# Optimization experiments

Hardware: AMD Instinct MI355X
Metric: run time of the kernel (lower is better)

Reference implementation:

```python
import jax, jax.numpy as jnp
import numpy as np

T = 2048          # sequence length
B = 1             # batch (forced by out.squeeze(1))
H = 2048          # hidden_size == input_size
L = 2             # num_layers
V = 128           # num_letters
TEMPERATURE = 1.0


def _lstm_layer(x, h0, c0, W_ih, W_hh, b_ih, b_hh):
    # x: [T, B, H_in], h0/c0: [B, H], W_ih: [4H, H_in], W_hh: [4H, H]
    b = b_ih + b_hh

    def step(carry, x_t):
        h, c = carry
        gates = x_t @ W_ih.T + h @ W_hh.T + b            # [B, 4H]
        i, f, g, o = jnp.split(gates, 4, axis=-1)        # torch gate order i,f,g,o
        i = jax.nn.sigmoid(i)
        f = jax.nn.sigmoid(f)
        g = jnp.tanh(g)
        o = jax.nn.sigmoid(o)
        c = f * c + i * g
        h = o * jnp.tanh(c)
        return (h, c), h

    (hT, cT), ys = jax.lax.scan(step, (h0, c0), x)       # ys: [T, B, H]
    return ys, hT, cT


def setup_inputs() -> dict:
    key = jax.random.key(0)
    ks = jax.random.split(key, 10)
    s = 1.0 / np.sqrt(H)  # torch default uniform init bound
    u = lambda k, shape: jax.random.uniform(k, shape, jnp.float32, -s, s)
    return {
        "x": jax.random.normal(ks[0], (T, B, H), jnp.float32),
        "h0": jnp.zeros((L, B, H), jnp.float32),
        "c0": jnp.zeros((L, B, H), jnp.float32),
        "W_ih": u(ks[1], (L, 4 * H, H)),
        "W_hh": u(ks[2], (L, 4 * H, H)),
        "b_ih": u(ks[3], (L, 4 * H)),
        "b_hh": u(ks[4], (L, 4 * H)),
        "fc_w": u(ks[5], (V, H)),
        "fc_b": u(ks[6], (V,)),
    }


def reference(x, h0, c0, W_ih, W_hh, b_ih, b_hh, fc_w, fc_b):
    out = x
    h_n, c_n = [], []
    for l in range(L):  # fixed small layer loop (dropout=0.1 is identity in eval)
        out, hT, cT = _lstm_layer(out, h0[l], c0[l], W_ih[l], W_hh[l], b_ih[l], b_hh[l])
        h_n.append(hT)
        c_n.append(cT)
    h_n = jnp.stack(h_n)
    c_n = jnp.stack(c_n)
    logits = out[:, 0, :] @ fc_w.T + fc_b                 # squeeze(1) -> [T, V]
    logp = jax.nn.log_softmax(logits / TEMPERATURE, axis=1)
    return logp, (h_n, c_n)
```

## Files before the change

### kernel.cpp

```cpp
#include <hip/hip_runtime.h>
#include <hip/hip_fp16.h>

#define T_LEN 2048
#define HID   2048
#define G4    8192
#define NV    128

typedef _Float16 h2_t __attribute__((ext_vector_type(2)));

__device__ __forceinline__ float uph(unsigned u) {
  return __half2float(__ushort_as_half((unsigned short)(u & 0xffffu)));
}
__device__ __forceinline__ unsigned pkh(float h, unsigned tag) {
  return (tag << 16) | (unsigned)__half_as_ushort(__float2half_rn(h));
}
__device__ __forceinline__ h2_t pk2(float a, float bb) {
  return __builtin_bit_cast(h2_t, __builtin_amdgcn_cvt_pkrtz(a, bb));
}

__device__ __forceinline__ uint4 ld_sc16(const unsigned* p) {
  uint4 r;
  asm volatile("global_load_dwordx4 %0, %1, off sc0 sc1\n\ts_waitcnt vmcnt(0)"
               : "=v"(r) : "v"(p) : "memory");
  return r;
}
__device__ __forceinline__ void ld_sc16x2(const unsigned* p0, const unsigned* p1,
                                          uint4& r0, uint4& r1) {
  asm volatile("global_load_dwordx4 %0, %2, off sc0 sc1\n\t"
               "global_load_dwordx4 %1, %3, off sc0 sc1\n\t"
               "s_waitcnt vmcnt(0)"
               : "=v"(r0), "=v"(r1) : "v"(p0), "v"(p1) : "memory");
}

__device__ __forceinline__ float fsigmoid(float x) {
  return __builtin_amdgcn_rcpf(1.f + __expf(-x));
}
__device__ __forceinline__ float ftanh(float x) {
  return 2.f * __builtin_amdgcn_rcpf(1.f + __expf(-2.f * x)) - 1.f;
}

__global__ __launch_bounds__(256, 2) void gemm_bias(
    const float* __restrict__ A, const float* __restrict__ B,
    const float* __restrict__ b1, const float* __restrict__ b2,
    float* __restrict__ C)
{
  const int N = 8192, K = 2048;
  __shared__ float As[32][68];
  __shared__ float Bs[32][68];
  const int tid = threadIdx.x;
  const int tx = tid & 15, ty = tid >> 4;
  const int row0 = blockIdx.y * 64, col0 = blockIdx.x * 64;
  const int lk = (tid & 7) * 4, lr = tid >> 3;
  float acc[4][4] = {};
  for (int k0 = 0; k0 < K; k0 += 32) {
    float4 a0 = *(const float4*)&A[(size_t)(row0 + lr)      * K + k0 + lk];
    float4 a1 = *(const float4*)&A[(size_t)(row0 + lr + 32) * K + k0 + lk];
    float4 bb0 = *(const float4*)&B[(size_t)(col0 + lr)      * K + k0 + lk];
    float4 bb1 = *(const float4*)&B[(size_t)(col0 + lr + 32) * K + k0 + lk];
    __syncthreads();
    As[lk+0][lr] = a0.x;  As[lk+1][lr] = a0.y;  As[lk+2][lr] = a0.z;  As[lk+3][lr] = a0.w;
    As[lk+0][lr+32] = a1.x; As[lk+1][lr+32] = a1.y; As[lk+2][lr+32] = a1.z; As[lk+3][lr+32] = a1.w;
    Bs[lk+0][lr] = bb0.x; Bs[lk+1][lr] = bb0.y; Bs[lk+2][lr] = bb0.z; Bs[lk+3][lr] = bb0.w;
    Bs[lk+0][lr+32] = bb1.x; Bs[lk+1][lr+32] = bb1.y; Bs[lk+2][lr+32] = bb1.z; Bs[lk+3][lr+32] = bb1.w;
    __syncthreads();
    #pragma unroll
    for (int kk = 0; kk < 32; ++kk) {
      float4 av = *(const float4*)&As[kk][ty * 4];
      float4 bv = *(const float4*)&Bs[kk][tx * 4];
      float am[4] = {av.x, av.y, av.z, av.w};
      float bm[4] = {bv.x, bv.y, bv.z, bv.w};
      #pragma unroll
      for (int i = 0; i < 4; ++i)
        #pragma unroll
        for (int j = 0; j < 4; ++j)
          acc[i][j] = fmaf(am[i], bm[j], acc[i][j]);
    }
  }
  #pragma unroll
  for (int i = 0; i < 4; ++i) {
    const int r = row0 + ty * 4 + i;
    #pragma unroll
    for (int j = 0; j < 4; ++j) {
      const int cc = col0 + tx * 4 + j;
      C[(size_t)r * N + cc] = acc[i][j] + b1[cc] + b2[cc];
    }
  }
}

__global__ __launch_bounds__(512, 2) void lstm_rec2(
    const float* __restrict__ Whh0,
    const float* __restrict__ Wih1,
    const float* __restrict__ Whh1,
    const float* __restrict__ G,
    const float* __restrict__ bih1, const float* __restrict__ bhh1,
    const float* __restrict__ h0v,
    const float* __restrict__ c0v,
    unsigned* HbufP0, unsigned* HbufP1,
    float* __restrict__ hn, float* __restrict__ cn)
{
  const int b = blockIdx.x;
  const int tid = threadIdx.x;
  const int w = tid >> 6;
  const int lane = tid & 63;
  const int j = b * 8 + w;
  __shared__ unsigned hs0[2][HID / 2];
  __shared__ unsigned hs1[2][HID / 2];

  h2_t wreg0[4][16], wregI[4][16], wregH[4][16];
  #pragma unroll
  for (int g = 0; g < 4; ++g) {
    const float* r0 = Whh0 + (size_t)(g * 2048 + j) * 2048 + 2 * lane;
    #pragma unroll
    for (int it = 0; it < 16; ++it) {
      float2 v = *(const float2*)(r0 + 128 * it);
      wreg0[g][it] = pk2(v.x, v.y);
    }
  }
  #pragma unroll
  for (int g = 0; g < 4; ++g) {
    const float* rI = Wih1 + (size_t)(g * 2048 + j) * 2048 + 2 * lane;
    #pragma unroll
    for (int it = 0; it < 16; ++it) {
      float2 v = *(const float2*)(rI + 128 * it);
      wregI[g][it] = pk2(v.x, v.y);
    }
  }
  #pragma unroll
  for (int g = 0; g < 4; ++g) {
    const float* rH = Whh1 + (size_t)(g * 2048 + j) * 2048 + 2 * lane;
    #pragma unroll
    for (int it = 0; it < 16; ++it) {
      float2 v = *(const float2*)(rH + 128 * it);
      wregH[g][it] = pk2(v.x, v.y);
    }
  }
  float bias1[4];
  #pragma unroll
  for (int g = 0; g < 4; ++g)
    bias1[g] = bih1[g * 2048 + j] + bhh1[g * 2048 + j];

  float c0val = c0v[j];
  float c1val = c0v[HID + j];
  float h0last = 0.f, h1last = 0.f;

  if (tid < 8) {
    __hip_atomic_store(&HbufP0[b * 8 + tid], pkh(h0v[b * 8 + tid], 0u),
                       __ATOMIC_RELAXED, __HIP_MEMORY_SCOPE_AGENT);
    __hip_atomic_store(&HbufP1[b * 8 + tid], pkh(h0v[HID + b * 8 + tid], 0u),
                       __ATOMIC_RELAXED, __HIP_MEMORY_SCOPE_AGENT);
  }

  for (int r = 1; r <= T_LEN + 1; ++r) {
    const bool doL0 = (r <= T_LEN);
    float gpre = (doL0 && lane < 4) ? G[(size_t)(r - 1) * G4 + lane * 2048 + j] : 0.f;

    const unsigned want0 = (unsigned)(r - 1);
    const unsigned* src0 = HbufP0 + (size_t)(r - 1) * HID + 4 * tid;
    uint4 u0, u1;
    if (r >= 2) {
      const unsigned want1 = (unsigned)(r - 2);
      const unsigned* src1 = HbufP1 + (size_t)(r - 2) * HID + 4 * tid;
      ld_sc16x2(src0, src1, u0, u1);
      int sp = 0;
      while (!(((u1.x >> 16) == want1) & ((u1.y >> 16) == want1) &
               ((u1.z >> 16) == want1) & ((u1.w >> 16) == want1))) {
        if (++sp > 4) __builtin_amdgcn_s_sleep(1);
        if (sp > (1 << 20)) break;
        u1 = ld_sc16(src1);
      }
      unsigned* row1 = hs1[r & 1];
      *(uint2*)&row1[2 * tid] = make_uint2((u1.x & 0xffffu) | (u1.y << 16),
                                           (u1.z & 0xffffu) | (u1.w << 16));
    } else {
      u0 = ld_sc16(src0);
    }
    {
      int sp = 0;
      while (!(((u0.x >> 16) == want0) & ((u0.y >> 16) == want0) &
               ((u0.z >> 16) == want0) & ((u0.w >> 16) == want0))) {
        if (++sp > 4) __builtin_amdgcn_s_sleep(1);
        if (sp > (1 << 20)) break;
        u0 = ld_sc16(src0);
      }
    }
    unsigned* row0 = hs0[r & 1];
    *(uint2*)&row0[2 * tid] = make_uint2((u0.x & 0xffffu) | (u0.y << 16),
                                         (u0.z & 0xffffu) | (u0.w << 16));
    __syncthreads();

    if (doL0) {
      const unsigned* hr = hs0[r & 1];
      float a0 = 0.f, a1 = 0.f, a2 = 0.f, a3 = 0.f;
      #pragma unroll
      for (int it = 0; it < 16; ++it) {
        h2_t hv = __builtin_bit_cast(h2_t, hr[lane + 64 * it]);
        a0 = __builtin_amdgcn_fdot2(wreg0[0][it], hv, a0, false);
        a1 = __builtin_amdgcn_fdot2(wreg0[1][it], hv, a1, false);
        a2 = __builtin_amdgcn_fdot2(wreg0[2][it], hv, a2, false);
        a3 = __builtin_amdgcn_fdot2(wreg0[3][it], hv, a3, false);
      }
      #pragma unroll
      for (int off = 32; off > 0; off >>= 1) {
        a0 += __shfl_xor(a0, off, 64);
        a1 += __shfl_xor(a1, off, 64);
        a2 += __shfl_xor(a2, off, 64);
        a3 += __shfl_xor(a3, off, 64);
      }
      float g0 = __shfl(gpre, 0, 64), g1 = __shfl(gpre, 1, 64);
      float g2 = __shfl(gpre, 2, 64), g3 = __shfl(gpre, 3, 64);
      float ig = fsigmoid(a0 + g0);
      float fg = fsigmoid(a1 + g1);
      float gg = ftanh(a2 + g2);
      float og = fsigmoid(a3 + g3);
      c0val = fg * c0val + ig * gg;
      h0last = og * ftanh(c0val);
      if (lane == 0)
        __hip_atomic_store(&HbufP0[(size_t)r * HID + j], pkh(h0last, (unsigned)r),
                           __ATOMIC_RELAXED, __HIP_MEMORY_SCOPE_AGENT);
    }

    if (r >= 2) {
      const unsigned* xr = hs0[r & 1];
      const unsigned* hr = hs1[r & 1];
      float a0 = 0.f, a1 = 0.f, a2 = 0.f, a3 = 0.f;
      #pragma unroll
      for (int it = 0; it < 16; ++it) {
        h2_t xv = __builtin_bit_cast(h2_t, xr[lane + 64 * it]);
        a0 = __builtin_amdgcn_fdot2(wregI[0][it], xv, a0, false);
        a1 = __builtin_amdgcn_fdot2(wregI[1][it], xv, a1, false);
        a2 = __builtin_amdgcn_fdot2(wregI[2][it], xv, a2, false);
        a3 = __builtin_amdgcn_fdot2(wregI[3][it], xv, a3, false);
        h2_t hv = __builtin_bit_cast(h2_t, hr[lane + 64 * it]);
        a0 = __builtin_amdgcn_fdot2(wregH[0][it], hv, a0, false);
        a1 = __builtin_amdgcn_fdot2(wregH[1][it], hv, a1, false);
        a2 = __builtin_amdgcn_fdot2(wregH[2][it], hv, a2, false);
        a3 = __builtin_amdgcn_fdot2(wregH[3][it], hv, a3, false);
      }
      #pragma unroll
      for (int off = 32; off > 0; off >>= 1) {
        a0 += __shfl_xor(a0, off, 64);
        a1 += __shfl_xor(a1, off, 64);
        a2 += __shfl_xor(a2, off, 64);
        a3 += __shfl_xor(a3, off, 64);
      }
      float ig = fsigmoid(a0 + bias1[0]);
      float fg = fsigmoid(a1 + bias1[1]);
      float gg = ftanh(a2 + bias1[2]);
      float og = fsigmoid(a3 + bias1[3]);
      c1val = fg * c1val + ig * gg;
      h1last = og * ftanh(c1val);
      if (lane == 0)
        __hip_atomic_store(&HbufP1[(size_t)(r - 1) * HID + j],
                           pkh(h1last, (unsigned)(r - 1)),
                           __ATOMIC_RELAXED, __HIP_MEMORY_SCOPE_AGENT);
    }
  }
  if (lane == 0) {
    hn[j] = h0last;       cn[j] = c0val;
    hn[HID + j] = h1last; cn[HID + j] = c1val;
  }
}

__global__ __launch_bounds__(128) void fc_lsm(
    const unsigned* __restrict__ Hrows,
    const float* __restrict__ fcw,
    const float* __restrict__ fcb,
    float* __restrict__ out)
{
  const int t = blockIdx.x;
  const int v = threadIdx.x;
  __shared__ float hs[HID];
  __shared__ float red[4];
  const unsigned* hrow = Hrows + (size_t)t * HID;
  for (int q = v; q < HID / 4; q += 128) {
    uint4 uv = *(const uint4*)&hrow[q * 4];
    hs[q * 4 + 0] = uph(uv.x); hs[q * 4 + 1] = uph(uv.y);
    hs[q * 4 + 2] = uph(uv.z); hs[q * 4 + 3] = uph(uv.w);
  }
  __syncthreads();
  const float* wrow = fcw + (size_t)v * HID;
  float acc = fcb[v];
  #pragma unroll 4
  for (int k = 0; k < HID; k += 4) {
    float4 wv = *(const float4*)&wrow[k];
    acc = fmaf(wv.x, hs[k],     acc);
    acc = fmaf(wv.y, hs[k + 1], acc);
    acc = fmaf(wv.z, hs[k + 2], acc);
    acc = fmaf(wv.w, hs[k + 3], acc);
  }
  float m = acc;
  #pragma unroll
  for (int off = 32; off > 0; off >>= 1) m = fmaxf(m, __shfl_xor(m, off, 64));
  if ((v & 63) == 0) red[v >> 6] = m;
  __syncthreads();
  m = fmaxf(red[0], red[1]);
  float e = expf(acc - m), s = e;
  #pragma unroll
  for (int off = 32; off > 0; off >>= 1) s += __shfl_xor(s, off, 64);
  if ((v & 63) == 0) red[2 + (v >> 6)] = s;
  __syncthreads();
  s = red[2] + red[3];
  out[(size_t)t * NV + v] = (acc - m) - logf(s);
}

extern "C" void kernel_launch(void* const* d_in, const int* in_sizes, int n_in,
                              void* d_out, int out_size, void* d_ws, size_t ws_size,
                              hipStream_t stream) {
  const float* x   = (const float*)d_in[0];
  const float* h0  = (const float*)d_in[1];
  const float* c0  = (const float*)d_in[2];
  const float* Wih = (const float*)d_in[3];
  const float* Whh = (const float*)d_in[4];
  const float* bih = (const float*)d_in[5];
  const float* bhh = (const float*)d_in[6];
  const float* fcw = (const float*)d_in[7];
  const float* fcb = (const float*)d_in[8];
  float* out = (float*)d_out;

  char* ws = (char*)d_ws;
  float*    G      = (float*)(ws);
  unsigned* HbufP0 = (unsigned*)(ws + 67108864);
  unsigned* HbufP1 = (unsigned*)(ws + 67108864 + 16785408);

  dim3 ggrid(G4 / 64, T_LEN / 64);

  gemm_bias<<<ggrid, 256, 0, stream>>>(x, Wih, bih, bhh, G);
  lstm_rec2<<<256, 512, 0, stream>>>(Whh, Wih + (size_t)G4 * HID,
                                     Whh + (size_t)G4 * HID, G,
                                     bih + G4, bhh + G4, h0, c0,
                                     HbufP0, HbufP1,
                                     out + 262144, out + 266240);
  fc_lsm<<<T_LEN, 128, 0, stream>>>(HbufP1 + HID, fcw, fcb, out);
}
```

Measured before the change: 12.08 ms.

## Replace per-element tagged hidden-state words with packed rows plus per-block flags

Each block now gathers its eight hidden values in shared memory and writes them as one packed fp16 row chunk, then sets a per-block flag word. Before, every value carried its own step tag in the upper half of a 32-bit word. Consumers poll 256 flags with one wavefront per layer and then bulk-load the packed rows, which halves the hidden-state traffic and drops per-element tag checks. In exchange it adds a flag-zeroing kernel, extra __syncthreads per step, and a store-then-flag ordering that relies on the waitcnt inside st_sc16.

```diff
diff --git a/kernel.cpp b/kernel.cpp
--- a/kernel.cpp
+++ b/kernel.cpp
@@ -7,12 +7,18 @@
 #define NV    128
 
 typedef _Float16 h2_t __attribute__((ext_vector_type(2)));
-
-__device__ __forceinline__ float uph(unsigned u) {
+typedef unsigned u32x4 __attribute__((ext_vector_type(4)));
+
+__device__ __forceinline__ float uplo(unsigned u) {
   return __half2float(__ushort_as_half((unsigned short)(u & 0xffffu)));
 }
-__device__ __forceinline__ unsigned pkh(float h, unsigned tag) {
-  return (tag << 16) | (unsigned)__half_as_ushort(__float2half_rn(h));
+__device__ __forceinline__ float uphi(unsigned u) {
+  return __half2float(__ushort_as_half((unsigned short)(u >> 16)));
+}
+__device__ __forceinline__ unsigned pku(float a, float b) {
+  unsigned lo = (unsigned)__half_as_ushort(__float2half_rn(a));
+  unsigned hi = (unsigned)__half_as_ushort(__float2half_rn(b));
+  return lo | (hi << 16);
 }
 __device__ __forceinline__ h2_t pk2(float a, float bb) {
   return __builtin_bit_cast(h2_t, __builtin_amdgcn_cvt_pkrtz(a, bb));
@@ -24,12 +30,13 @@
                : "=v"(r) : "v"(p) : "memory");
   return r;
 }
-__device__ __forceinline__ void ld_sc16x2(const unsigned* p0, const unsigned* p1,
-                                          uint4& r0, uint4& r1) {
-  asm volatile("global_load_dwordx4 %0, %2, off sc0 sc1\n\t"
-               "global_load_dwordx4 %1, %3, off sc0 sc1\n\t"
-               "s_waitcnt vmcnt(0)"
-               : "=v"(r0), "=v"(r1) : "v"(p0), "v"(p1) : "memory");
+__device__ __forceinline__ void st_sc16(unsigned* p, u32x4 v) {
+  asm volatile("global_store_dwordx4 %0, %1, off sc0 sc1\n\ts_waitcnt vmcnt(0)"
+               :: "v"(p), "v"(v) : "memory");
+}
+__device__ __forceinline__ void st_sc4(unsigned* p, unsigned v) {
+  asm volatile("global_store_dword %0, %1, off sc0 sc1"
+               :: "v"(p), "v"(v) : "memory");
 }
 
 __device__ __forceinline__ float fsigmoid(float x) {
@@ -37,6 +44,25 @@
 }
 __device__ __forceinline__ float ftanh(float x) {
   return 2.f * __builtin_amdgcn_rcpf(1.f + __expf(-2.f * x)) - 1.f;
+}
+
+__device__ __forceinline__ void poll_flags(const unsigned* f, unsigned want,
+                                           int lane) {
+  const unsigned* p = f + 4 * lane;
+  int sp = 0;
+  for (;;) {
+    uint4 u = ld_sc16(p);
+    bool ok = (u.x == want) & (u.y == want) & (u.z == want) & (u.w == want);
+    if (__all(ok)) break;
+    if (++sp > 8) __builtin_amdgcn_s_sleep(1);
+    if (sp > (1 << 15)) break;
+  }
+}
+
+__global__ __launch_bounds__(256) void zero_flags(unsigned* f, int n4) {
+  u32x4 z = {0u, 0u, 0u, 0u};
+  for (int i = blockIdx.x * 256 + threadIdx.x; i < n4; i += gridDim.x * 256)
+    st_sc16(f + 4 * (size_t)i, z);
 }
 
 __global__ __launch_bounds__(256, 2) void gemm_bias(
@@ -87,7 +113,7 @@
   }
 }
 
-__global__ __launch_bounds__(512, 2) void lstm_rec2(
+__global__ __launch_bounds__(512) void lstm_rec2(
     const float* __restrict__ Whh0,
     const float* __restrict__ Wih1,
     const float* __restrict__ Whh1,
@@ -95,7 +121,8 @@
     const float* __restrict__ bih1, const float* __restrict__ bhh1,
     const float* __restrict__ h0v,
     const float* __restrict__ c0v,
-    unsigned* HbufP0, unsigned* HbufP1,
+    unsigned* Hrow0, unsigned* Hrow1,
+    unsigned* flags0, unsigned* flags1,
     float* __restrict__ hn, float* __restrict__ cn)
 {
   const int b = blockIdx.x;
@@ -105,6 +132,7 @@
   const int j = b * 8 + w;
   __shared__ unsigned hs0[2][HID / 2];
   __shared__ unsigned hs1[2][HID / 2];
+  __shared__ float hloc0[8], hloc1[8];
 
   h2_t wreg0[4][16], wregI[4][16], wregH[4][16];
   #pragma unroll
@@ -143,49 +171,40 @@
   float c1val = c0v[HID + j];
   float h0last = 0.f, h1last = 0.f;
 
-  if (tid < 8) {
-    __hip_atomic_store(&HbufP0[b * 8 + tid], pkh(h0v[b * 8 + tid], 0u),
-                       __ATOMIC_RELAXED, __HIP_MEMORY_SCOPE_AGENT);
-    __hip_atomic_store(&HbufP1[b * 8 + tid], pkh(h0v[HID + b * 8 + tid], 0u),
-                       __ATOMIC_RELAXED, __HIP_MEMORY_SCOPE_AGENT);
+  if (tid == 0) {
+    u32x4 P = {pku(h0v[b*8+0], h0v[b*8+1]),
+               pku(h0v[b*8+2], h0v[b*8+3]),
+               pku(h0v[b*8+4], h0v[b*8+5]),
+               pku(h0v[b*8+6], h0v[b*8+7])};
+    st_sc16(Hrow0 + b * 4, P);
+    st_sc4(flags0 + b, 1u);
+  }
+  if (tid == 64) {
+    u32x4 P = {pku(h0v[HID+b*8+0], h0v[HID+b*8+1]),
+               pku(h0v[HID+b*8+2], h0v[HID+b*8+3]),
+               pku(h0v[HID+b*8+4], h0v[HID+b*8+5]),
+               pku(h0v[HID+b*8+6], h0v[HID+b*8+7])};
+    st_sc16(Hrow1 + b * 4, P);
+    st_sc4(flags1 + b, 1u);
   }
 
   for (int r = 1; r <= T_LEN + 1; ++r) {
     const bool doL0 = (r <= T_LEN);
+    const bool doL1 = (r >= 2);
     float gpre = (doL0 && lane < 4) ? G[(size_t)(r - 1) * G4 + lane * 2048 + j] : 0.f;
 
-    const unsigned want0 = (unsigned)(r - 1);
-    const unsigned* src0 = HbufP0 + (size_t)(r - 1) * HID + 4 * tid;
-    uint4 u0, u1;
-    if (r >= 2) {
-      const unsigned want1 = (unsigned)(r - 2);
-      const unsigned* src1 = HbufP1 + (size_t)(r - 2) * HID + 4 * tid;
-      ld_sc16x2(src0, src1, u0, u1);
-      int sp = 0;
-      while (!(((u1.x >> 16) == want1) & ((u1.y >> 16) == want1) &
-               ((u1.z >> 16) == want1) & ((u1.w >> 16) == want1))) {
-        if (++sp > 4) __builtin_amdgcn_s_sleep(1);
-        if (sp > (1 << 20)) break;
-        u1 = ld_sc16(src1);
-      }
-      unsigned* row1 = hs1[r & 1];
-      *(uint2*)&row1[2 * tid] = make_uint2((u1.x & 0xffffu) | (u1.y << 16),
-                                           (u1.z & 0xffffu) | (u1.w << 16));
-    } else {
-      u0 = ld_sc16(src0);
-    }
-    {
-      int sp = 0;
-      while (!(((u0.x >> 16) == want0) & ((u0.y >> 16) == want0) &
-               ((u0.z >> 16) == want0) & ((u0.w >> 16) == want0))) {
-        if (++sp > 4) __builtin_amdgcn_s_sleep(1);
-        if (sp > (1 << 20)) break;
-        u0 = ld_sc16(src0);
-      }
-    }
-    unsigned* row0 = hs0[r & 1];
-    *(uint2*)&row0[2 * tid] = make_uint2((u0.x & 0xffffu) | (u0.y << 16),
-                                         (u0.z & 0xffffu) | (u0.w << 16));
+    if (w == 0)        poll_flags(flags0 + (size_t)(r - 1) * 256, (unsigned)r, lane);
+    else if (w == 1 && doL1) poll_flags(flags1 + (size_t)(r - 2) * 256, (unsigned)(r - 1), lane);
+    __syncthreads();
+
+    if (tid < 256) {
+      uint4 u = ld_sc16(Hrow0 + (size_t)(r - 1) * 1024 + 4 * tid);
+      *(uint4*)&hs0[r & 1][4 * tid] = u;
+    } else if (doL1) {
+      const int q = tid - 256;
+      uint4 u = ld_sc16(Hrow1 + (size_t)(r - 2) * 1024 + 4 * q);
+      *(uint4*)&hs1[r & 1][4 * q] = u;
+    }
     __syncthreads();
 
     if (doL0) {
@@ -214,12 +233,17 @@
       float og = fsigmoid(a3 + g3);
       c0val = fg * c0val + ig * gg;
       h0last = og * ftanh(c0val);
-      if (lane == 0)
-        __hip_atomic_store(&HbufP0[(size_t)r * HID + j], pkh(h0last, (unsigned)r),
-                           __ATOMIC_RELAXED, __HIP_MEMORY_SCOPE_AGENT);
-    }
-
-    if (r >= 2) {
+      if (lane == 0) hloc0[w] = h0last;
+    }
+    __syncthreads();
+    if (doL0 && tid == 0) {
+      u32x4 P = {pku(hloc0[0], hloc0[1]), pku(hloc0[2], hloc0[3]),
+                 pku(hloc0[4], hloc0[5]), pku(hloc0[6], hloc0[7])};
+      st_sc16(Hrow0 + (size_t)r * 1024 + b * 4, P);
+      st_sc4(flags0 + (size_t)r * 256 + b, (unsigned)(r + 1));
+    }
+
+    if (doL1) {
       const unsigned* xr = hs0[r & 1];
       const unsigned* hr = hs1[r & 1];
       float a0 = 0.f, a1 = 0.f, a2 = 0.f, a3 = 0.f;
@@ -249,10 +273,14 @@
       float og = fsigmoid(a3 + bias1[3]);
       c1val = fg * c1val + ig * gg;
       h1last = og * ftanh(c1val);
-      if (lane == 0)
-        __hip_atomic_store(&HbufP1[(size_t)(r - 1) * HID + j],
-                           pkh(h1last, (unsigned)(r - 1)),
-                           __ATOMIC_RELAXED, __HIP_MEMORY_SCOPE_AGENT);
+      if (lane == 0) hloc1[w] = h1last;
+    }
+    __syncthreads();
+    if (doL1 && tid == 64) {
+      u32x4 P = {pku(hloc1[0], hloc1[1]), pku(hloc1[2], hloc1[3]),
+                 pku(hloc1[4], hloc1[5]), pku(hloc1[6], hloc1[7])};
+      st_sc16(Hrow1 + (size_t)(r - 1) * 1024 + b * 4, P);
+      st_sc4(flags1 + (size_t)(r - 1) * 256 + b, (unsigned)r);
     }
   }
   if (lane == 0) {
@@ -271,11 +299,13 @@
   const int v = threadIdx.x;
   __shared__ float hs[HID];
   __shared__ float red[4];
-  const unsigned* hrow = Hrows + (size_t)t * HID;
-  for (int q = v; q < HID / 4; q += 128) {
+  const unsigned* hrow = Hrows + (size_t)t * 1024;
+  for (int q = v; q < 256; q += 128) {
     uint4 uv = *(const uint4*)&hrow[q * 4];
-    hs[q * 4 + 0] = uph(uv.x); hs[q * 4 + 1] = uph(uv.y);
-    hs[q * 4 + 2] = uph(uv.z); hs[q * 4 + 3] = uph(uv.w);
+    hs[q*8+0] = uplo(uv.x); hs[q*8+1] = uphi(uv.x);
+    hs[q*8+2] = uplo(uv.y); hs[q*8+3] = uphi(uv.y);
+    hs[q*8+4] = uplo(uv.z); hs[q*8+5] = uphi(uv.z);
+    hs[q*8+6] = uplo(uv.w); hs[q*8+7] = uphi(uv.w);
   }
   __syncthreads();
   const float* wrow = fcw + (size_t)v * HID;
@@ -319,8 +349,13 @@
 
   char* ws = (char*)d_ws;
   float*    G      = (float*)(ws);
-  unsigned* HbufP0 = (unsigned*)(ws + 67108864);
-  unsigned* HbufP1 = (unsigned*)(ws + 67108864 + 16785408);
+  unsigned* Hrow0  = (unsigned*)(ws + 67108864);
+  unsigned* Hrow1  = (unsigned*)(ws + 67108864 + 8392704);
+  unsigned* flags0 = (unsigned*)(ws + 67108864 + 2 * 8392704);
+  unsigned* flags1 = (unsigned*)(ws + 67108864 + 2 * 8392704 + 2098176);
+
+  const int nflag4 = (2 * 2098176) / 16;
+  zero_flags<<<256, 256, 0, stream>>>(flags0, nflag4);
 
   dim3 ggrid(G4 / 64, T_LEN / 64);
 
@@ -328,7 +363,7 @@
   lstm_rec2<<<256, 512, 0, stream>>>(Whh, Wih + (size_t)G4 * HID,
                                      Whh + (size_t)G4 * HID, G,
                                      bih + G4, bhh + G4, h0, c0,
-                                     HbufP0, HbufP1,
+                                     Hrow0, Hrow1, flags0, flags1,
                                      out + 262144, out + 266240);
-  fc_lsm<<<T_LEN, 128, 0, stream>>>(HbufP1 + HID, fcw, fcb, out);
-}
+  fc_lsm<<<T_LEN, 128, 0, stream>>>(Hrow1 + 1024, fcw, fcb, out);
+}
```

Measured after the change: 13.43 ms. 1.11x slower.
